# Performance work log

Hardware: AMD Instinct MI355X
Metric: run time of the kernel (lower is better)

The kernel has to match this reference:

```python
import jax, jax.numpy as jnp
import numpy as np

B, T, I, H = 512, 256, 256, 512

def setup_inputs() -> dict:
    key = jax.random.key(0)
    k1, k2, k3, k4, k5 = jax.random.split(key, 5)
    s = 1.0 / np.sqrt(H + I)
    return {
        "x": jax.random.normal(k1, (B, T, I), dtype=jnp.float32),
        "W_w": jax.random.normal(k2, (4 * H, H + I), dtype=jnp.float32) * s,
        "W_b": jax.random.normal(k3, (4 * H,), dtype=jnp.float32) * s,
        "fc_w": jax.random.normal(k4, (1, H), dtype=jnp.float32) * (1.0 / np.sqrt(H)),
        "fc_b": jax.random.normal(k5, (1,), dtype=jnp.float32) * 0.02,
    }

def reference(x, W_w, W_b, fc_w, fc_b):
    # combined = cat(h_prev, x_t): first H columns of W_w act on h, last I on x
    Wh = W_w[:, :H]          # [4H, H]
    Wx = W_w[:, H:]          # [4H, I]
    # precompute input contributions for all timesteps: [B, T, 4H]
    xW = jnp.einsum('bti,gi->btg', x, Wx) + W_b

    def step(carry, xw_t):
        h, c = carry
        gates = xw_t + h @ Wh.T                      # [B, 4H]
        f, i, o, c_hat = jnp.split(gates, 4, axis=1)  # chunk order f,i,o,c_hat
        f = jax.nn.sigmoid(f)
        i = jax.nn.sigmoid(i)
        o = jax.nn.sigmoid(o)
        c_hat = jnp.tanh(c_hat)
        c_new = f * c + i * c_hat
        h_new = o * jnp.tanh(c_new)
        return (h_new, c_new), None

    h0 = jnp.zeros((x.shape[0], H), dtype=x.dtype)
    c0 = jnp.zeros((x.shape[0], H), dtype=x.dtype)
    (h_T, _), _ = jax.lax.scan(step, (h0, c0), jnp.swapaxes(xW, 0, 1))
    return h_T @ fc_w.T + fc_b                       # [B, 1]
```

## Files before the change

### kernel.cpp

```cpp
#include <hip/hip_runtime.h>
#include <hip/hip_bf16.h>
#include <stdint.h>


#define B_SZ 512
#define T_SZ 256
#define I_SZ 256
#define H_SZ 512
#define K_SZ 768
#define BH   (B_SZ * H_SZ)

typedef float  f32x4  __attribute__((ext_vector_type(4)));
typedef __bf16 bf16x8 __attribute__((ext_vector_type(8)));

__device__ __forceinline__ float fast_sigmoid(float v) {
  return __builtin_amdgcn_rcpf(1.0f + __expf(-v));
}
__device__ __forceinline__ float fast_tanh(float v) {
  return 1.0f - 2.0f * __builtin_amdgcn_rcpf(1.0f + __expf(2.0f * v));
}

#define HLOAD(dst, off) \
  asm volatile("global_load_dwordx4 %0, %1, off offset:" off " sc0 sc1" \
               : "=v"(dst) : "v"(hsrc) : "memory")
#define HSTORE(off, val) \
  asm volatile("global_store_short %0, %1, off offset:" off " sc0 sc1" \
               :: "v"(hdst), "v"(val) : "memory")

__global__ __launch_bounds__(256, 1)
void lstm_persist(const float* __restrict__ x,
                  const float* __restrict__ Ww,
                  const float* __restrict__ Wb,
                  __bf16* __restrict__ hbuf,
                  float* __restrict__ hf32,
                  unsigned int* __restrict__ flags)
{
  __shared__ bf16x8 bw[96 * 64];

  const int wg    = blockIdx.x;
  const int chunk = wg & 7;
  const int jb    = wg >> 3;
  const int tid   = threadIdx.x;
  const int wv    = tid >> 6;
  const int ln    = tid & 63;
  const int l16   = ln & 15;
  const int lhi   = ln >> 4;

  const int colW = jb * 16 + l16;

  for (int c = wv; c < 96; c += 4) {
    const int kt = c >> 2;
    const int nt = c & 3;
    const int k0 = kt * 32 + lhi * 8;
    const int g  = nt * 512 + colW;
    const float* wr = Ww + (size_t)g * K_SZ + k0;
    const float4 w0 = *(const float4*)(wr);
    const float4 w1 = *(const float4*)(wr + 4);
    bf16x8 v;
    v[0]=(__bf16)w0.x; v[1]=(__bf16)w0.y; v[2]=(__bf16)w0.z; v[3]=(__bf16)w0.w;
    v[4]=(__bf16)w1.x; v[5]=(__bf16)w1.y; v[6]=(__bf16)w1.z; v[7]=(__bf16)w1.w;
    bw[c * 64 + ln] = v;
  }

  const float bias0 = Wb[0 * 512 + colW];
  const float bias1 = Wb[1 * 512 + colW];
  const float bias2 = Wb[2 * 512 + colW];
  const float bias3 = Wb[3 * 512 + colW];

  __syncthreads();

  float cst[4] = {0.f, 0.f, 0.f, 0.f};

  const int rowA = chunk * 64 + wv * 16 + l16;
  const int rowD = chunk * 64 + wv * 16 + lhi * 4;
  const float* xrow = x + (size_t)rowA * T_SZ * I_SZ + lhi * 8;
  unsigned int* cnt = flags + (chunk * 4 + wv) * 32;

  float4 xp0[8], xp1[8];
  {
    const float* xr = xrow;
#pragma unroll
    for (int kt = 0; kt < 8; ++kt) {
      xp0[kt] = *(const float4*)(xr + kt * 32);
      xp1[kt] = *(const float4*)(xr + kt * 32 + 4);
    }
  }

  bf16x8 hf[16];

  for (int t = 0; t < T_SZ; ++t) {
    if (t > 0) {
      const unsigned target = 32u * (unsigned)t;
      while (__hip_atomic_load(cnt, __ATOMIC_RELAXED,
                               __HIP_MEMORY_SCOPE_AGENT) < target) { }
      const __bf16* hsrc = hbuf + (size_t)(t & 1) * BH
                                + (size_t)rowA * H_SZ + lhi * 8;
      HLOAD(hf[0],  "0");   HLOAD(hf[1],  "64");  HLOAD(hf[2],  "128");
      HLOAD(hf[3],  "192"); HLOAD(hf[4],  "256"); HLOAD(hf[5],  "320");
      HLOAD(hf[6],  "384"); HLOAD(hf[7],  "448"); HLOAD(hf[8],  "512");
      HLOAD(hf[9],  "576"); HLOAD(hf[10], "640"); HLOAD(hf[11], "704");
      HLOAD(hf[12], "768"); HLOAD(hf[13], "832"); HLOAD(hf[14], "896");
      HLOAD(hf[15], "960");
    }

    f32x4 acc0 = {0.f,0.f,0.f,0.f}, acc1 = {0.f,0.f,0.f,0.f};
    f32x4 acc2 = {0.f,0.f,0.f,0.f}, acc3 = {0.f,0.f,0.f,0.f};

#pragma unroll
    for (int kt = 0; kt < 8; ++kt) {
      bf16x8 a;
      a[0]=(__bf16)xp0[kt].x; a[1]=(__bf16)xp0[kt].y;
      a[2]=(__bf16)xp0[kt].z; a[3]=(__bf16)xp0[kt].w;
      a[4]=(__bf16)xp1[kt].x; a[5]=(__bf16)xp1[kt].y;
      a[6]=(__bf16)xp1[kt].z; a[7]=(__bf16)xp1[kt].w;
      const int cb = (16 + kt) * 4;
      acc0 = __builtin_amdgcn_mfma_f32_16x16x32_bf16(a, bw[(cb+0)*64 + ln], acc0, 0, 0, 0);
      acc1 = __builtin_amdgcn_mfma_f32_16x16x32_bf16(a, bw[(cb+1)*64 + ln], acc1, 0, 0, 0);
      acc2 = __builtin_amdgcn_mfma_f32_16x16x32_bf16(a, bw[(cb+2)*64 + ln], acc2, 0, 0, 0);
      acc3 = __builtin_amdgcn_mfma_f32_16x16x32_bf16(a, bw[(cb+3)*64 + ln], acc3, 0, 0, 0);
    }

    if (t > 0) {
      asm volatile("s_waitcnt vmcnt(0)" ::: "memory");
      __builtin_amdgcn_sched_barrier(0);
#pragma unroll
      for (int kt = 0; kt < 16; ++kt) {
        const int cb = kt * 4;
        acc0 = __builtin_amdgcn_mfma_f32_16x16x32_bf16(hf[kt], bw[(cb+0)*64 + ln], acc0, 0, 0, 0);
        acc1 = __builtin_amdgcn_mfma_f32_16x16x32_bf16(hf[kt], bw[(cb+1)*64 + ln], acc1, 0, 0, 0);
        acc2 = __builtin_amdgcn_mfma_f32_16x16x32_bf16(hf[kt], bw[(cb+2)*64 + ln], acc2, 0, 0, 0);
        acc3 = __builtin_amdgcn_mfma_f32_16x16x32_bf16(hf[kt], bw[(cb+3)*64 + ln], acc3, 0, 0, 0);
      }
    }

    float hnv[4];
#pragma unroll
    for (int r = 0; r < 4; ++r) {
      const float fg = fast_sigmoid(acc0[r] + bias0);
      const float ig = fast_sigmoid(acc1[r] + bias1);
      const float og = fast_sigmoid(acc2[r] + bias2);
      const float gg = fast_tanh(acc3[r] + bias3);
      const float cn = fg * cst[r] + ig * gg;
      cst[r] = cn;
      hnv[r] = og * fast_tanh(cn);
    }

    if (t < T_SZ - 1) {
      __bf16* hdst = hbuf + (size_t)((t + 1) & 1) * BH
                          + (size_t)rowD * H_SZ + colW;
      const unsigned u0 = __builtin_bit_cast(unsigned short, (__bf16)hnv[0]);
      const unsigned u1 = __builtin_bit_cast(unsigned short, (__bf16)hnv[1]);
      const unsigned u2 = __builtin_bit_cast(unsigned short, (__bf16)hnv[2]);
      const unsigned u3 = __builtin_bit_cast(unsigned short, (__bf16)hnv[3]);
      HSTORE("0",    u0);
      HSTORE("1024", u1);
      HSTORE("2048", u2);
      HSTORE("3072", u3);
      asm volatile("s_waitcnt vmcnt(0)" ::: "memory");
      if (ln == 0)
        __hip_atomic_fetch_add(cnt, 1u, __ATOMIC_RELAXED,
                               __HIP_MEMORY_SCOPE_AGENT);
      const float* xr = xrow + (size_t)(t + 1) * I_SZ;
#pragma unroll
      for (int kt = 0; kt < 8; ++kt) {
        xp0[kt] = *(const float4*)(xr + kt * 32);
        xp1[kt] = *(const float4*)(xr + kt * 32 + 4);
      }
    } else {
#pragma unroll
      for (int r = 0; r < 4; ++r)
        hf32[(size_t)(rowD + r) * H_SZ + colW] = hnv[r];
    }
  }
}

__global__ __launch_bounds__(256)
void fc_head(const float* __restrict__ hf32, const float* __restrict__ fcw,
             const float* __restrict__ fcb, float* __restrict__ out)
{
  const int b = blockIdx.x * 256 + threadIdx.x;
  if (b >= B_SZ) return;
  const float4* hp = (const float4*)(hf32 + (size_t)b * H_SZ);
  const float4* wp = (const float4*)fcw;
  float s = 0.f;
#pragma unroll 8
  for (int j = 0; j < H_SZ / 4; ++j) {
    const float4 h = hp[j];
    const float4 w = wp[j];
    s += h.x * w.x + h.y * w.y + h.z * w.z + h.w * w.w;
  }
  out[b] = s + fcb[0];
}

extern "C" void kernel_launch(void* const* d_in, const int* in_sizes, int n_in,
                              void* d_out, int out_size, void* d_ws, size_t ws_size,
                              hipStream_t stream) {
  const float* x   = (const float*)d_in[0];
  const float* Ww  = (const float*)d_in[1];
  const float* Wb  = (const float*)d_in[2];
  const float* fcw = (const float*)d_in[3];
  const float* fcb = (const float*)d_in[4];
  float* out = (float*)d_out;

  char* ws = (char*)d_ws;
  unsigned int* flags = (unsigned int*)ws;
  __bf16* hbuf = (__bf16*)(ws + 4096);
  float*  hf32 = (float*)(ws + 4096 + (size_t)2 * BH * sizeof(__bf16));

  hipMemsetAsync(ws, 0, 4096, stream);

  lstm_persist<<<256, 256, 0, stream>>>(x, Ww, Wb, hbuf, hf32, flags);
  fc_head<<<2, 256, 0, stream>>>(hf32, fcw, fcb, out);
}
```

Measured before the change: 1.835 ms.

## Replace atomic counter with per-producer flag slots and precompute next-step x-projection

Replaces the shared atomic fetch-add counter with per-producer flag words: each of 32 producers stores its step index to its own slot, and consumers poll all 32 slots in one wave-wide load. This removes atomic contention on a single counter from the step-to-step critical path. The x-projection MFMAs for step t+1 now run right after publishing h_t, into a second accumulator set, so only the h-dependent MFMAs remain after the wait. The cost is extra accumulator registers and more polling traffic.

```diff
diff --git a/kernel.cpp b/kernel.cpp
--- a/kernel.cpp
+++ b/kernel.cpp
@@ -52,8 +52,7 @@
     const int kt = c >> 2;
     const int nt = c & 3;
     const int k0 = kt * 32 + lhi * 8;
-    const int g  = nt * 512 + colW;
-    const float* wr = Ww + (size_t)g * K_SZ + k0;
+    const float* wr = Ww + (size_t)(nt * 512 + colW) * K_SZ + k0;
     const float4 w0 = *(const float4*)(wr);
     const float4 w1 = *(const float4*)(wr + 4);
     bf16x8 v;
@@ -69,85 +68,78 @@
 
   __syncthreads();
 
-  float cst[4] = {0.f, 0.f, 0.f, 0.f};
-
   const int rowA = chunk * 64 + wv * 16 + l16;
   const int rowD = chunk * 64 + wv * 16 + lhi * 4;
-  const float* xrow = x + (size_t)rowA * T_SZ * I_SZ + lhi * 8;
-  unsigned int* cnt = flags + (chunk * 4 + wv) * 32;
-
-  float4 xp0[8], xp1[8];
-  {
-    const float* xr = xrow;
-#pragma unroll
-    for (int kt = 0; kt < 8; ++kt) {
-      xp0[kt] = *(const float4*)(xr + kt * 32);
-      xp1[kt] = *(const float4*)(xr + kt * 32 + 4);
-    }
-  }
-
-  bf16x8 hf[16];
-
-  for (int t = 0; t < T_SZ; ++t) {
+  const float* xlane = x + (size_t)rowA * T_SZ * I_SZ + lhi * 8;
+  unsigned int* fbase = flags + (chunk * 4 + wv) * 32;
+  const unsigned int* fspin = fbase + (ln & 31);
+  unsigned int* fq = fbase + jb;
+  __bf16* hb0 = hbuf;
+  __bf16* hb1 = hbuf + BH;
+
+  float cst[4] = {0.f, 0.f, 0.f, 0.f};
+
+  auto xpart = [&](f32x4 (&accN)[4], int tn) {
+#pragma unroll
+    for (int nt = 0; nt < 4; ++nt) accN[nt] = (f32x4){0.f, 0.f, 0.f, 0.f};
+    const float* xr = xlane + (size_t)tn * I_SZ;
+#pragma unroll
+    for (int q = 0; q < 8; ++q) {
+      const float4 a0 = *(const float4*)(xr + q * 32);
+      const float4 a1 = *(const float4*)(xr + q * 32 + 4);
+      bf16x8 a;
+      a[0]=(__bf16)a0.x; a[1]=(__bf16)a0.y; a[2]=(__bf16)a0.z; a[3]=(__bf16)a0.w;
+      a[4]=(__bf16)a1.x; a[5]=(__bf16)a1.y; a[6]=(__bf16)a1.z; a[7]=(__bf16)a1.w;
+#pragma unroll
+      for (int nt = 0; nt < 4; ++nt)
+        accN[nt] = __builtin_amdgcn_mfma_f32_16x16x32_bf16(
+                     a, bw[((16 + q) * 4 + nt) * 64 + ln], accN[nt], 0, 0, 0);
+    }
+  };
+
+  auto step = [&](f32x4 (&acc)[4], f32x4 (&accN)[4], int t) {
     if (t > 0) {
-      const unsigned target = 32u * (unsigned)t;
-      while (__hip_atomic_load(cnt, __ATOMIC_RELAXED,
-                               __HIP_MEMORY_SCOPE_AGENT) < target) { }
-      const __bf16* hsrc = hbuf + (size_t)(t & 1) * BH
-                                + (size_t)rowA * H_SZ + lhi * 8;
+      unsigned fv;
+      do {
+        asm volatile("global_load_dword %0, %1, off sc0 sc1\n\t"
+                     "s_waitcnt vmcnt(0)"
+                     : "=v"(fv) : "v"(fspin) : "memory");
+      } while (__any((int)(fv < (unsigned)t)));
+
+      const __bf16* hsrc = ((t & 1) ? hb1 : hb0)
+                           + (size_t)rowA * H_SZ + lhi * 8;
+      bf16x8 hf[16];
       HLOAD(hf[0],  "0");   HLOAD(hf[1],  "64");  HLOAD(hf[2],  "128");
       HLOAD(hf[3],  "192"); HLOAD(hf[4],  "256"); HLOAD(hf[5],  "320");
       HLOAD(hf[6],  "384"); HLOAD(hf[7],  "448"); HLOAD(hf[8],  "512");
       HLOAD(hf[9],  "576"); HLOAD(hf[10], "640"); HLOAD(hf[11], "704");
       HLOAD(hf[12], "768"); HLOAD(hf[13], "832"); HLOAD(hf[14], "896");
       HLOAD(hf[15], "960");
-    }
-
-    f32x4 acc0 = {0.f,0.f,0.f,0.f}, acc1 = {0.f,0.f,0.f,0.f};
-    f32x4 acc2 = {0.f,0.f,0.f,0.f}, acc3 = {0.f,0.f,0.f,0.f};
-
-#pragma unroll
-    for (int kt = 0; kt < 8; ++kt) {
-      bf16x8 a;
-      a[0]=(__bf16)xp0[kt].x; a[1]=(__bf16)xp0[kt].y;
-      a[2]=(__bf16)xp0[kt].z; a[3]=(__bf16)xp0[kt].w;
-      a[4]=(__bf16)xp1[kt].x; a[5]=(__bf16)xp1[kt].y;
-      a[6]=(__bf16)xp1[kt].z; a[7]=(__bf16)xp1[kt].w;
-      const int cb = (16 + kt) * 4;
-      acc0 = __builtin_amdgcn_mfma_f32_16x16x32_bf16(a, bw[(cb+0)*64 + ln], acc0, 0, 0, 0);
-      acc1 = __builtin_amdgcn_mfma_f32_16x16x32_bf16(a, bw[(cb+1)*64 + ln], acc1, 0, 0, 0);
-      acc2 = __builtin_amdgcn_mfma_f32_16x16x32_bf16(a, bw[(cb+2)*64 + ln], acc2, 0, 0, 0);
-      acc3 = __builtin_amdgcn_mfma_f32_16x16x32_bf16(a, bw[(cb+3)*64 + ln], acc3, 0, 0, 0);
-    }
-
-    if (t > 0) {
       asm volatile("s_waitcnt vmcnt(0)" ::: "memory");
       __builtin_amdgcn_sched_barrier(0);
 #pragma unroll
       for (int kt = 0; kt < 16; ++kt) {
-        const int cb = kt * 4;
-        acc0 = __builtin_amdgcn_mfma_f32_16x16x32_bf16(hf[kt], bw[(cb+0)*64 + ln], acc0, 0, 0, 0);
-        acc1 = __builtin_amdgcn_mfma_f32_16x16x32_bf16(hf[kt], bw[(cb+1)*64 + ln], acc1, 0, 0, 0);
-        acc2 = __builtin_amdgcn_mfma_f32_16x16x32_bf16(hf[kt], bw[(cb+2)*64 + ln], acc2, 0, 0, 0);
-        acc3 = __builtin_amdgcn_mfma_f32_16x16x32_bf16(hf[kt], bw[(cb+3)*64 + ln], acc3, 0, 0, 0);
+#pragma unroll
+        for (int nt = 0; nt < 4; ++nt)
+          acc[nt] = __builtin_amdgcn_mfma_f32_16x16x32_bf16(
+                      hf[kt], bw[(kt * 4 + nt) * 64 + ln], acc[nt], 0, 0, 0);
       }
     }
 
     float hnv[4];
 #pragma unroll
     for (int r = 0; r < 4; ++r) {
-      const float fg = fast_sigmoid(acc0[r] + bias0);
-      const float ig = fast_sigmoid(acc1[r] + bias1);
-      const float og = fast_sigmoid(acc2[r] + bias2);
-      const float gg = fast_tanh(acc3[r] + bias3);
+      const float fg = fast_sigmoid(acc[0][r] + bias0);
+      const float ig = fast_sigmoid(acc[1][r] + bias1);
+      const float og = fast_sigmoid(acc[2][r] + bias2);
+      const float gg = fast_tanh(acc[3][r] + bias3);
       const float cn = fg * cst[r] + ig * gg;
       cst[r] = cn;
       hnv[r] = og * fast_tanh(cn);
     }
 
     if (t < T_SZ - 1) {
-      __bf16* hdst = hbuf + (size_t)((t + 1) & 1) * BH
-                          + (size_t)rowD * H_SZ + colW;
+      __bf16* hdst = ((t & 1) ? hb0 : hb1) + (size_t)rowD * H_SZ + colW;
       const unsigned u0 = __builtin_bit_cast(unsigned short, (__bf16)hnv[0]);
       const unsigned u1 = __builtin_bit_cast(unsigned short, (__bf16)hnv[1]);
       const unsigned u2 = __builtin_bit_cast(unsigned short, (__bf16)hnv[2]);
@@ -157,20 +149,24 @@
       HSTORE("2048", u2);
       HSTORE("3072", u3);
       asm volatile("s_waitcnt vmcnt(0)" ::: "memory");
-      if (ln == 0)
-        __hip_atomic_fetch_add(cnt, 1u, __ATOMIC_RELAXED,
-                               __HIP_MEMORY_SCOPE_AGENT);
-      const float* xr = xrow + (size_t)(t + 1) * I_SZ;
-#pragma unroll
-      for (int kt = 0; kt < 8; ++kt) {
-        xp0[kt] = *(const float4*)(xr + kt * 32);
-        xp1[kt] = *(const float4*)(xr + kt * 32 + 4);
+      if (ln == 0) {
+        const unsigned tv = (unsigned)(t + 1);
+        asm volatile("global_store_dword %0, %1, off sc0 sc1"
+                     :: "v"(fq), "v"(tv) : "memory");
       }
+      xpart(accN, t + 1);
     } else {
 #pragma unroll
       for (int r = 0; r < 4; ++r)
         hf32[(size_t)(rowD + r) * H_SZ + colW] = hnv[r];
     }
+  };
+
+  f32x4 accA[4], accB[4];
+  xpart(accA, 0);
+  for (int t2 = 0; t2 < T_SZ; t2 += 2) {
+    step(accA, accB, t2);
+    step(accB, accA, t2 + 1);
   }
 }
 
```

New measurement: 2.107 ms. +14.9%, slower.
